# Kernel optimization log

Hardware: AMD Instinct MI355X
Metric: run time of the kernel (lower is better)

Reference implementation:

```python
import jax, jax.numpy as jnp
import numpy as np

NEG_SLOPE = 0.2
EPS = 1e-16


def add_self_loops(edge_index, num_nodes):
    loops = jnp.arange(num_nodes, dtype=edge_index.dtype)
    loops = jnp.stack([loops, loops])  # [2, N]
    return jnp.concatenate([edge_index, loops], axis=1)


def gat_conv(x, edge_index, W, att_src, att_dst, bias, heads, out_c, concat):
    # x: [N, F_in]; edge_index: [2, E] (src row 0 -> dst row 1)
    N = x.shape[0]
    h = (x @ W).reshape(N, heads, out_c)            # [N, H, C]
    src, dst = edge_index[0], edge_index[1]
    a_src = (h * att_src).sum(-1)                    # [N, H]
    a_dst = (h * att_dst).sum(-1)                    # [N, H]
    e = a_src[src] + a_dst[dst]                      # [E, H]
    e = jnp.where(e > 0, e, NEG_SLOPE * e)           # leaky_relu
    # segment softmax over destination node
    m = jax.ops.segment_max(e, dst, num_segments=N)  # [N, H]
    ex = jnp.exp(e - m[dst])                         # [E, H]
    denom = jax.ops.segment_sum(ex, dst, num_segments=N)  # [N, H]
    alpha = ex / (denom[dst] + EPS)                  # [E, H]
    msg = alpha[:, :, None] * h[src]                 # [E, H, C]
    out = jax.ops.segment_sum(msg, dst, num_segments=N)   # [N, H, C]
    if concat:
        out = out.reshape(N, heads * out_c)
    else:
        out = out.mean(axis=1)
    return out + bias


def setup_inputs() -> dict:
    key = jax.random.key(0)
    ks = jax.random.split(key, 12)
    N, E, F_IN, HID, H1, OUT = 100000, 1600000, 512, 8, 8, 40
    x = jax.random.normal(ks[0], (N, F_IN), dtype=jnp.float32)
    edge_index = jax.random.randint(ks[1], (2, E), 0, N, dtype=jnp.int64)
    glorot = lambda k, shp: jax.random.normal(k, shp, jnp.float32) * jnp.sqrt(2.0 / (shp[0] + shp[-1]))
    W1 = glorot(ks[2], (F_IN, H1 * HID))
    att_src1 = glorot(ks[3], (H1, HID))
    att_dst1 = glorot(ks[4], (H1, HID))
    b1 = jnp.zeros((H1 * HID,), jnp.float32)
    W2 = glorot(ks[5], (H1 * HID, 1 * OUT))
    att_src2 = glorot(ks[6], (1, OUT))
    att_dst2 = glorot(ks[7], (1, OUT))
    b2 = jnp.zeros((OUT,), jnp.float32)
    return {"x": x, "edge_index": edge_index, "W1": W1, "att_src1": att_src1,
            "att_dst1": att_dst1, "b1": b1, "W2": W2, "att_src2": att_src2,
            "att_dst2": att_dst2, "b2": b2}


def reference(x, edge_index, W1, att_src1, att_dst1, b1, W2, att_src2, att_dst2, b2):
    N = x.shape[0]
    ei = add_self_loops(edge_index, N)
    h = gat_conv(x, ei, W1, att_src1, att_dst1, b1, heads=8, out_c=8, concat=True)
    h = jax.nn.relu(h)
    # dropout p=0.0 / eval mode -> identity
    out = gat_conv(h, ei, W2, att_src2, att_dst2, b2, heads=1, out_c=40, concat=False)
    return jax.nn.log_softmax(out, axis=1)
```

## Files before the change

kernel.cpp:

```cpp
#include <hip/hip_runtime.h>
#include <math.h>

#define NEG_SLOPE 0.2f
#define EPS_DEN 1e-16f

__device__ __forceinline__ float leaky(float v) { return v > 0.f ? v : NEG_SLOPE * v; }

typedef __attribute__((ext_vector_type(8))) short bf16x8;
typedef __attribute__((ext_vector_type(4))) float f32x4;

__device__ __forceinline__ unsigned bf16rne(float f) {
    unsigned u = __float_as_uint(f);
    return (u + 0x7FFFu + ((u >> 16) & 1u)) >> 16;
}
__device__ __forceinline__ unsigned pack2(float a, float b) {
    unsigned r;
    asm("v_cvt_pk_bf16_f32 %0, %1, %2" : "=v"(r) : "v"(a), "v"(b));
    return r;
}
__device__ __forceinline__ float bfu(unsigned short u) {
    return __uint_as_float(((unsigned)u) << 16);
}

__global__ __launch_bounds__(256) void gemm1_mfma(
    const float* __restrict__ x, const float* __restrict__ W1,
    const float* __restrict__ att_src1, const float* __restrict__ att_dst1,
    unsigned short* __restrict__ h1b, float* __restrict__ a_src,
    float* __restrict__ a_dst, int N)
{
    __shared__ __align__(16) unsigned short As[128 * 40];
    __shared__ __align__(16) unsigned short Bs[64 * 40];

    const int t = threadIdx.x;
    const int w = t >> 6;
    const int lane = t & 63;
    const int m16 = lane & 15;
    const int quad = lane >> 4;
    const int rowBase = blockIdx.x * 128;

    f32x4 acc[2][4];
#pragma unroll
    for (int i = 0; i < 2; ++i)
#pragma unroll
        for (int j = 0; j < 4; ++j) acc[i][j] = (f32x4){0.f, 0.f, 0.f, 0.f};

    const float4* x4 = (const float4*)x;

#pragma unroll 1
    for (int chunk = 0; chunk < 16; ++chunk) {
        const int k0 = chunk * 32;
#pragma unroll
        for (int r = 0; r < 4; ++r) {
            int e = t + r * 256;
            int row = e >> 3;
            int kg = e & 7;
            int grow = rowBase + row;
            float4 v = make_float4(0.f, 0.f, 0.f, 0.f);
            if (grow < N) v = x4[(size_t)grow * 128 + (k0 >> 2) + kg];
            uint2 pk = make_uint2(pack2(v.x, v.y), pack2(v.z, v.w));
            *(uint2*)&As[row * 40 + kg * 4] = pk;
        }
        {
            int c = lane;
            int jb = w * 8;
            float f[8];
#pragma unroll
            for (int j = 0; j < 8; ++j) f[j] = W1[(size_t)(k0 + jb + j) * 64 + c];
            uint4 pk;
            pk.x = pack2(f[0], f[1]); pk.y = pack2(f[2], f[3]);
            pk.z = pack2(f[4], f[5]); pk.w = pack2(f[6], f[7]);
            *(uint4*)&Bs[c * 40 + jb] = pk;
        }
        __syncthreads();
        bf16x8 a0 = *(const bf16x8*)&As[(w * 32 + m16) * 40 + quad * 8];
        bf16x8 a1 = *(const bf16x8*)&As[(w * 32 + 16 + m16) * 40 + quad * 8];
#pragma unroll
        for (int j = 0; j < 4; ++j) {
            bf16x8 b = *(const bf16x8*)&Bs[(j * 16 + m16) * 40 + quad * 8];
            acc[0][j] = __builtin_amdgcn_mfma_f32_16x16x32_bf16(a0, b, acc[0][j], 0, 0, 0);
            acc[1][j] = __builtin_amdgcn_mfma_f32_16x16x32_bf16(a1, b, acc[1][j], 0, 0, 0);
        }
        __syncthreads();
    }

    float ats[4], atd[4];
#pragma unroll
    for (int j = 0; j < 4; ++j) {
        ats[j] = att_src1[j * 16 + m16];
        atd[j] = att_dst1[j * 16 + m16];
    }

#pragma unroll
    for (int i = 0; i < 2; ++i)
#pragma unroll
        for (int reg = 0; reg < 4; ++reg) {
            int r = rowBase + w * 32 + i * 16 + quad * 4 + reg;
            if (r < N) {
#pragma unroll
                for (int j = 0; j < 4; ++j) {
                    float val = acc[i][j][reg];
                    h1b[(size_t)r * 64 + j * 16 + m16] = (unsigned short)bf16rne(val);
                    float ps = val * ats[j];
                    float pd = val * atd[j];
                    ps += __shfl_xor(ps, 1); pd += __shfl_xor(pd, 1);
                    ps += __shfl_xor(ps, 2); pd += __shfl_xor(pd, 2);
                    ps += __shfl_xor(ps, 4); pd += __shfl_xor(pd, 4);
                    if ((m16 & 7) == 0) {
                        int head = j * 2 + (m16 >> 3);
                        a_src[(size_t)r * 8 + head] = ps;
                        a_dst[(size_t)r * 8 + head] = pd;
                    }
                }
            }
        }
}

__global__ __launch_bounds__(256) void deg_kernel(
    const int* __restrict__ ei, unsigned* __restrict__ deg, int E, int Etot)
{
    int idx = blockIdx.x * blockDim.x + threadIdx.x;
    if (idx >= Etot) return;
    int d = (idx < E) ? ei[E + idx] : (idx - E);
    atomicAdd(&deg[d], 1u);
}

__global__ __launch_bounds__(256) void scanA_kernel(
    const unsigned* __restrict__ deg, unsigned* __restrict__ loc,
    unsigned* __restrict__ bsum, int N)
{
    __shared__ unsigned sh[256];
    int i = blockIdx.x * 256 + threadIdx.x;
    unsigned v = (i < N) ? deg[i] : 0u;
    sh[threadIdx.x] = v;
    __syncthreads();
    for (int off = 1; off < 256; off <<= 1) {
        unsigned u = (threadIdx.x >= (unsigned)off) ? sh[threadIdx.x - off] : 0u;
        __syncthreads();
        sh[threadIdx.x] += u;
        __syncthreads();
    }
    if (i < N) loc[i] = sh[threadIdx.x] - v;
    if (threadIdx.x == 255) bsum[blockIdx.x] = sh[255];
}

__global__ __launch_bounds__(1024) void scanB_kernel(unsigned* __restrict__ bsum, int nb)
{
    __shared__ unsigned sh[1024];
    int t = threadIdx.x;
    unsigned carry = 0;
    for (int base = 0; base < nb; base += 1024) {
        int i = base + t;
        unsigned v = (i < nb) ? bsum[i] : 0u;
        sh[t] = v;
        __syncthreads();
        for (int off = 1; off < 1024; off <<= 1) {
            unsigned u = (t >= off) ? sh[t - off] : 0u;
            __syncthreads();
            sh[t] += u;
            __syncthreads();
        }
        unsigned incl = sh[t];
        unsigned tot  = sh[1023];
        __syncthreads();
        if (i < nb) bsum[i] = incl - v + carry;
        carry += tot;
        __syncthreads();
    }
}

__global__ __launch_bounds__(256) void scanC_kernel(
    const unsigned* __restrict__ loc, const unsigned* __restrict__ bsum,
    unsigned* __restrict__ rowstart, unsigned* __restrict__ cursor, int N, int Etot)
{
    int i = blockIdx.x * 256 + threadIdx.x;
    if (i >= N) return;
    unsigned r = loc[i] + bsum[blockIdx.x];
    rowstart[i] = r;
    cursor[i] = r;
    if (i == 0) rowstart[N] = (unsigned)Etot;
}

__global__ __launch_bounds__(256) void scatter_kernel(
    const int* __restrict__ ei, unsigned* __restrict__ cursor,
    int* __restrict__ csr_src, int E, int Etot, int sliceW)
{
    int slice = blockIdx.x & 7;
    int idx = (blockIdx.x >> 3) * 256 + threadIdx.x;
    if (idx >= Etot) return;
    int d = (idx < E) ? ei[E + idx] : (idx - E);
    int lo = slice * sliceW;
    if (d < lo || d >= lo + sliceW) return;
    int s = (idx < E) ? ei[idx] : d;
    unsigned pos = atomicAdd(&cursor[d], 1u);
    csr_src[pos] = s;
}

__global__ __launch_bounds__(256) void aggr1_kernel(
    const unsigned* __restrict__ rowstart, const int* __restrict__ csr_src,
    const float* __restrict__ a_src, const float* __restrict__ a_dst,
    const unsigned short* __restrict__ h1b, const float* __restrict__ b1,
    float* __restrict__ h2, int N)
{
    int g = blockIdx.x * 4 + (threadIdx.x >> 6);
    int lane = threadIdx.x & 63;
    if (g >= N) return;
    int half = lane >> 5;
    int l = lane & 31;
    int h = l >> 2;
    float ad = a_dst[(size_t)g * 8 + h];
    const unsigned* h1u = (const unsigned*)h1b;
    unsigned k0 = rowstart[g], k1 = rowstart[g + 1];
    float ax0 = 0.f, ay0 = 0.f, ax1 = 0.f, ay1 = 0.f;
    float dn0 = 0.f, dn1 = 0.f;
    unsigned k = k0;
    for (; k + 4 <= k1; k += 4) {
        int e0 = k + half, e1 = k + 2 + half;
        int s0 = csr_src[e0], s1 = csr_src[e1];
        float p0 = __expf(leaky(a_src[(size_t)s0 * 8 + h] + ad));
        float p1 = __expf(leaky(a_src[(size_t)s1 * 8 + h] + ad));
        unsigned v0 = h1u[(size_t)s0 * 32 + l];
        unsigned v1 = h1u[(size_t)s1 * 32 + l];
        ax0 += p0 * bfu((unsigned short)v0); ay0 += p0 * bfu((unsigned short)(v0 >> 16)); dn0 += p0;
        ax1 += p1 * bfu((unsigned short)v1); ay1 += p1 * bfu((unsigned short)(v1 >> 16)); dn1 += p1;
    }
    for (; k < k1; k += 2) {
        unsigned e = k + half;
        if (e < k1) {
            int s = csr_src[e];
            float p = __expf(leaky(a_src[(size_t)s * 8 + h] + ad));
            unsigned v = h1u[(size_t)s * 32 + l];
            ax0 += p * bfu((unsigned short)v); ay0 += p * bfu((unsigned short)(v >> 16)); dn0 += p;
        }
    }
    float ax = ax0 + ax1, ay = ay0 + ay1, dn = dn0 + dn1;
    ax += __shfl_xor(ax, 32);
    ay += __shfl_xor(ay, 32);
    dn += __shfl_xor(dn, 32);
    if (half == 0) {
        float inv = 1.f / (dn + EPS_DEN);
        float vx = ax * inv + b1[2 * l];
        float vy = ay * inv + b1[2 * l + 1];
        float2 o;
        o.x = vx > 0.f ? vx : 0.f;
        o.y = vy > 0.f ? vy : 0.f;
        *(float2*)&h2[(size_t)g * 64 + 2 * l] = o;
    }
}

__global__ __launch_bounds__(256) void gemm2_kernel(
    const float* __restrict__ h2, const float* __restrict__ W2,
    const float* __restrict__ att_src2, const float* __restrict__ att_dst2,
    unsigned short* __restrict__ h3b32, unsigned short* __restrict__ h3b8,
    float* __restrict__ a_src, float* __restrict__ a_dst, int N)
{
    __shared__ float Wl[64 * 40];
    int t = threadIdx.x;
    for (int i = t; i < 64 * 40; i += 256) Wl[i] = W2[i];
    __syncthreads();
    int lane = t & 63, wy = t >> 6;
    int row = blockIdx.x * 4 + wy;
    if (row >= N) return;
    float acc = 0.f;
    const float* hr = h2 + (size_t)row * 64;
    if (lane < 40) {
#pragma unroll 8
        for (int k = 0; k < 64; ++k) acc += hr[k] * Wl[k * 40 + lane];
        if (lane < 32) h3b32[(size_t)row * 32 + lane] = (unsigned short)bf16rne(acc);
        else           h3b8[(size_t)row * 8 + (lane - 32)] = (unsigned short)bf16rne(acc);
    }
    float ps = (lane < 40) ? acc * att_src2[lane] : 0.f;
    float pd = (lane < 40) ? acc * att_dst2[lane] : 0.f;
#pragma unroll
    for (int off = 32; off; off >>= 1) { ps += __shfl_down(ps, off); pd += __shfl_down(pd, off); }
    if (lane == 0) { a_src[row] = ps; a_dst[row] = pd; }
}

__global__ __launch_bounds__(256) void aggr2_kernel(
    const unsigned* __restrict__ rowstart, const int* __restrict__ csr_src,
    const float* __restrict__ a_src, const float* __restrict__ a_dst,
    const unsigned short* __restrict__ h3b32, const unsigned short* __restrict__ h3b8,
    const float* __restrict__ b2, float* __restrict__ y, int N)
{
    int g = blockIdx.x * 4 + (threadIdx.x >> 6);
    int lane = threadIdx.x & 63;
    if (g >= N) return;
    int half = lane >> 5;
    int l = lane & 31;
    const bool valid = l < 20;
    const unsigned* hsrc = (l < 16) ? (const unsigned*)h3b32 : (const unsigned*)h3b8;
    const int rowmul = (l < 16) ? 16 : 4;
    const int cidx   = (l < 16) ? l : (valid ? l - 16 : 0);
    float ad = a_dst[g];
    unsigned k0 = rowstart[g], k1 = rowstart[g + 1];
    float ax0 = 0.f, ay0 = 0.f, ax1 = 0.f, ay1 = 0.f;
    float dn0 = 0.f, dn1 = 0.f;
    unsigned k = k0;
    for (; k + 4 <= k1; k += 4) {
        int e0 = k + half, e1 = k + 2 + half;
        int s0 = csr_src[e0], s1 = csr_src[e1];
        float p0 = __expf(leaky(a_src[s0] + ad));
        float p1 = __expf(leaky(a_src[s1] + ad));
        unsigned v0 = valid ? hsrc[(size_t)s0 * rowmul + cidx] : 0u;
        unsigned v1 = valid ? hsrc[(size_t)s1 * rowmul + cidx] : 0u;
        ax0 += p0 * bfu((unsigned short)v0); ay0 += p0 * bfu((unsigned short)(v0 >> 16)); dn0 += p0;
        ax1 += p1 * bfu((unsigned short)v1); ay1 += p1 * bfu((unsigned short)(v1 >> 16)); dn1 += p1;
    }
    for (; k < k1; k += 2) {
        unsigned e = k + half;
        if (e < k1) {
            int s = csr_src[e];
            float p = __expf(leaky(a_src[s] + ad));
            unsigned v = valid ? hsrc[(size_t)s * rowmul + cidx] : 0u;
            ax0 += p * bfu((unsigned short)v); ay0 += p * bfu((unsigned short)(v >> 16)); dn0 += p;
        }
    }
    float ax = ax0 + ax1, ay = ay0 + ay1, dn = dn0 + dn1;
    ax += __shfl_xor(ax, 32);
    ay += __shfl_xor(ay, 32);
    dn += __shfl_xor(dn, 32);
    float inv = 1.f / (dn + EPS_DEN);
    float vx = valid ? (ax * inv + b2[2 * l]) : -INFINITY;
    float vy = valid ? (ay * inv + b2[2 * l + 1]) : -INFINITY;
    float mx = fmaxf(vx, vy);
#pragma unroll
    for (int off = 16; off; off >>= 1) mx = fmaxf(mx, __shfl_xor(mx, off));
    float ex = valid ? (__expf(vx - mx) + __expf(vy - mx)) : 0.f;
    float ss = ex;
#pragma unroll
    for (int off = 16; off; off >>= 1) ss += __shfl_xor(ss, off);
    float lse = mx + __logf(ss);
    if (half == 0 && valid) {
        float2 o;
        o.x = vx - lse;
        o.y = vy - lse;
        *(float2*)&y[(size_t)g * 40 + 2 * l] = o;
    }
}

extern "C" void kernel_launch(void* const* d_in, const int* in_sizes, int n_in,
                              void* d_out, int out_size, void* d_ws, size_t ws_size,
                              hipStream_t stream)
{
    const float* x        = (const float*)d_in[0];
    const int*   ei       = (const int*)d_in[1];
    const float* W1       = (const float*)d_in[2];
    const float* att_src1 = (const float*)d_in[3];
    const float* att_dst1 = (const float*)d_in[4];
    const float* b1       = (const float*)d_in[5];
    const float* W2       = (const float*)d_in[6];
    const float* att_src2 = (const float*)d_in[7];
    const float* att_dst2 = (const float*)d_in[8];
    const float* b2       = (const float*)d_in[9];
    float* y = (float*)d_out;

    int N = in_sizes[0] / 512;
    int E = in_sizes[1] / 2;
    int Etot = E + N;
    int nb = (N + 255) / 256;
    int sliceW = (N + 7) / 8;

    char* p = (char*)d_ws;
    unsigned short* h1b = (unsigned short*)p; p += (size_t)N * 64 * 2;
    float* a_src1a  = (float*)p;   p += (size_t)N * 8 * 4;
    float* a_dst1a  = (float*)p;   p += (size_t)N * 8 * 4;
    float* h2       = (float*)p;   p += (size_t)N * 64 * 4;
    unsigned short* h3b32 = (unsigned short*)p; p += (size_t)N * 32 * 2;
    unsigned short* h3b8  = (unsigned short*)p; p += (size_t)N * 8 * 2;
    float* a_src2a  = (float*)p;   p += (size_t)N * 4;
    float* a_dst2a  = (float*)p;   p += (size_t)N * 4;
    unsigned* deg   = (unsigned*)p; p += (size_t)N * 4;
    unsigned* loc   = (unsigned*)p; p += (size_t)N * 4;
    unsigned* bsum  = (unsigned*)p; p += (size_t)nb * 4;
    unsigned* rowstart = (unsigned*)p; p += (size_t)(N + 1) * 4;
    unsigned* cursor   = (unsigned*)p; p += (size_t)N * 4;
    int* csr_src    = (int*)p;     p += (size_t)Etot * 4;

    hipMemsetAsync(deg, 0, (size_t)N * 4, stream);

    gemm1_mfma<<<(N + 127) / 128, 256, 0, stream>>>(x, W1, att_src1, att_dst1, h1b, a_src1a, a_dst1a, N);

    deg_kernel<<<(Etot + 255) / 256, 256, 0, stream>>>(ei, deg, E, Etot);
    scanA_kernel<<<nb, 256, 0, stream>>>(deg, loc, bsum, N);
    scanB_kernel<<<1, 1024, 0, stream>>>(bsum, nb);
    scanC_kernel<<<nb, 256, 0, stream>>>(loc, bsum, rowstart, cursor, N, Etot);
    scatter_kernel<<<8 * ((Etot + 255) / 256), 256, 0, stream>>>(ei, cursor, csr_src, E, Etot, sliceW);

    aggr1_kernel<<<(N + 3) / 4, 256, 0, stream>>>(rowstart, csr_src, a_src1a, a_dst1a, h1b, b1, h2, N);

    gemm2_kernel<<<(N + 3) / 4, 256, 0, stream>>>(h2, W2, att_src2, att_dst2, h3b32, h3b8, a_src2a, a_dst2a, N);

    aggr2_kernel<<<(N + 3) / 4, 256, 0, stream>>>(rowstart, csr_src, a_src2a, a_dst2a, h3b32, h3b8, b2, y, N);
}
```

Before: 679.1 us.

## Prefetch next GEMM1 chunk into registers and unroll aggregation loops deeper

GEMM1 now loads the next K-chunk of x and W1 into registers while the MFMAs for the current chunk run, a register-level software pipeline meant to hide global load latency. Both aggregation kernels unroll the edge loop to 8 edges (4 per half-wave) with extra independent accumulators, so more gathers are in flight. Index arithmetic switches from 64-bit size_t to 32-bit unsigned to cut address computation cost. The costs are higher register pressure, possible lower occupancy, and a slightly different float summation order.

```diff
diff --git a/kernel.cpp b/kernel.cpp
--- a/kernel.cpp
+++ b/kernel.cpp
@@ -45,33 +45,56 @@
         for (int j = 0; j < 4; ++j) acc[i][j] = (f32x4){0.f, 0.f, 0.f, 0.f};
 
     const float4* x4 = (const float4*)x;
+    const int jb = w * 8;
+    const int c = lane;
+
+    int arow[4], akg[4], agrow[4];
+    bool aok[4];
+#pragma unroll
+    for (int r = 0; r < 4; ++r) {
+        int e = t + r * 256;
+        arow[r] = e >> 3;
+        akg[r] = e & 7;
+        agrow[r] = rowBase + arow[r];
+        aok[r] = agrow[r] < N;
+    }
+
+    float4 vx[4];
+    float wf[8];
+
+#pragma unroll
+    for (int r = 0; r < 4; ++r) {
+        vx[r] = make_float4(0.f, 0.f, 0.f, 0.f);
+        if (aok[r]) vx[r] = x4[(size_t)agrow[r] * 128 + akg[r]];
+    }
+#pragma unroll
+    for (int j = 0; j < 8; ++j) wf[j] = W1[(size_t)(jb + j) * 64 + c];
 
 #pragma unroll 1
     for (int chunk = 0; chunk < 16; ++chunk) {
-        const int k0 = chunk * 32;
 #pragma unroll
         for (int r = 0; r < 4; ++r) {
-            int e = t + r * 256;
-            int row = e >> 3;
-            int kg = e & 7;
-            int grow = rowBase + row;
-            float4 v = make_float4(0.f, 0.f, 0.f, 0.f);
-            if (grow < N) v = x4[(size_t)grow * 128 + (k0 >> 2) + kg];
-            uint2 pk = make_uint2(pack2(v.x, v.y), pack2(v.z, v.w));
-            *(uint2*)&As[row * 40 + kg * 4] = pk;
+            uint2 pk = make_uint2(pack2(vx[r].x, vx[r].y), pack2(vx[r].z, vx[r].w));
+            *(uint2*)&As[arow[r] * 40 + akg[r] * 4] = pk;
         }
         {
-            int c = lane;
-            int jb = w * 8;
-            float f[8];
-#pragma unroll
-            for (int j = 0; j < 8; ++j) f[j] = W1[(size_t)(k0 + jb + j) * 64 + c];
             uint4 pk;
-            pk.x = pack2(f[0], f[1]); pk.y = pack2(f[2], f[3]);
-            pk.z = pack2(f[4], f[5]); pk.w = pack2(f[6], f[7]);
+            pk.x = pack2(wf[0], wf[1]); pk.y = pack2(wf[2], wf[3]);
+            pk.z = pack2(wf[4], wf[5]); pk.w = pack2(wf[6], wf[7]);
             *(uint4*)&Bs[c * 40 + jb] = pk;
         }
         __syncthreads();
+
+        if (chunk < 15) {
+            const int k0n = (chunk + 1) * 32;
+#pragma unroll
+            for (int r = 0; r < 4; ++r) {
+                if (aok[r]) vx[r] = x4[(size_t)agrow[r] * 128 + (k0n >> 2) + akg[r]];
+            }
+#pragma unroll
+            for (int j = 0; j < 8; ++j) wf[j] = W1[(size_t)(k0n + jb + j) * 64 + c];
+        }
+
         bf16x8 a0 = *(const bf16x8*)&As[(w * 32 + m16) * 40 + quad * 8];
         bf16x8 a1 = *(const bf16x8*)&As[(w * 32 + 16 + m16) * 40 + quad * 8];
 #pragma unroll
@@ -211,15 +234,34 @@
     const unsigned* h1u = (const unsigned*)h1b;
     unsigned k0 = rowstart[g], k1 = rowstart[g + 1];
     float ax0 = 0.f, ay0 = 0.f, ax1 = 0.f, ay1 = 0.f;
-    float dn0 = 0.f, dn1 = 0.f;
+    float ax2 = 0.f, ay2 = 0.f, ax3 = 0.f, ay3 = 0.f;
+    float dn0 = 0.f, dn1 = 0.f, dn2 = 0.f, dn3 = 0.f;
     unsigned k = k0;
+    for (; k + 8 <= k1; k += 8) {
+        int s0 = csr_src[k + half];
+        int s1 = csr_src[k + 2 + half];
+        int s2 = csr_src[k + 4 + half];
+        int s3 = csr_src[k + 6 + half];
+        float p0 = __expf(leaky(a_src[(unsigned)s0 * 8u + h] + ad));
+        float p1 = __expf(leaky(a_src[(unsigned)s1 * 8u + h] + ad));
+        float p2 = __expf(leaky(a_src[(unsigned)s2 * 8u + h] + ad));
+        float p3 = __expf(leaky(a_src[(unsigned)s3 * 8u + h] + ad));
+        unsigned v0 = h1u[(unsigned)s0 * 32u + l];
+        unsigned v1 = h1u[(unsigned)s1 * 32u + l];
+        unsigned v2 = h1u[(unsigned)s2 * 32u + l];
+        unsigned v3 = h1u[(unsigned)s3 * 32u + l];
+        ax0 += p0 * bfu((unsigned short)v0); ay0 += p0 * bfu((unsigned short)(v0 >> 16)); dn0 += p0;
+        ax1 += p1 * bfu((unsigned short)v1); ay1 += p1 * bfu((unsigned short)(v1 >> 16)); dn1 += p1;
+        ax2 += p2 * bfu((unsigned short)v2); ay2 += p2 * bfu((unsigned short)(v2 >> 16)); dn2 += p2;
+        ax3 += p3 * bfu((unsigned short)v3); ay3 += p3 * bfu((unsigned short)(v3 >> 16)); dn3 += p3;
+    }
     for (; k + 4 <= k1; k += 4) {
-        int e0 = k + half, e1 = k + 2 + half;
-        int s0 = csr_src[e0], s1 = csr_src[e1];
-        float p0 = __expf(leaky(a_src[(size_t)s0 * 8 + h] + ad));
-        float p1 = __expf(leaky(a_src[(size_t)s1 * 8 + h] + ad));
-        unsigned v0 = h1u[(size_t)s0 * 32 + l];
-        unsigned v1 = h1u[(size_t)s1 * 32 + l];
+        int s0 = csr_src[k + half];
+        int s1 = csr_src[k + 2 + half];
+        float p0 = __expf(leaky(a_src[(unsigned)s0 * 8u + h] + ad));
+        float p1 = __expf(leaky(a_src[(unsigned)s1 * 8u + h] + ad));
+        unsigned v0 = h1u[(unsigned)s0 * 32u + l];
+        unsigned v1 = h1u[(unsigned)s1 * 32u + l];
         ax0 += p0 * bfu((unsigned short)v0); ay0 += p0 * bfu((unsigned short)(v0 >> 16)); dn0 += p0;
         ax1 += p1 * bfu((unsigned short)v1); ay1 += p1 * bfu((unsigned short)(v1 >> 16)); dn1 += p1;
     }
@@ -227,12 +269,14 @@
         unsigned e = k + half;
         if (e < k1) {
             int s = csr_src[e];
-            float p = __expf(leaky(a_src[(size_t)s * 8 + h] + ad));
-            unsigned v = h1u[(size_t)s * 32 + l];
+            float p = __expf(leaky(a_src[(unsigned)s * 8u + h] + ad));
+            unsigned v = h1u[(unsigned)s * 32u + l];
             ax0 += p * bfu((unsigned short)v); ay0 += p * bfu((unsigned short)(v >> 16)); dn0 += p;
         }
     }
-    float ax = ax0 + ax1, ay = ay0 + ay1, dn = dn0 + dn1;
+    float ax = (ax0 + ax1) + (ax2 + ax3);
+    float ay = (ay0 + ay1) + (ay2 + ay3);
+    float dn = (dn0 + dn1) + (dn2 + dn3);
     ax += __shfl_xor(ax, 32);
     ay += __shfl_xor(ay, 32);
     dn += __shfl_xor(dn, 32);
@@ -288,20 +332,39 @@
     int l = lane & 31;
     const bool valid = l < 20;
     const unsigned* hsrc = (l < 16) ? (const unsigned*)h3b32 : (const unsigned*)h3b8;
-    const int rowmul = (l < 16) ? 16 : 4;
-    const int cidx   = (l < 16) ? l : (valid ? l - 16 : 0);
+    const unsigned rowmul = (l < 16) ? 16u : 4u;
+    const unsigned cidx   = (l < 16) ? (unsigned)l : (valid ? (unsigned)(l - 16) : 0u);
     float ad = a_dst[g];
     unsigned k0 = rowstart[g], k1 = rowstart[g + 1];
     float ax0 = 0.f, ay0 = 0.f, ax1 = 0.f, ay1 = 0.f;
-    float dn0 = 0.f, dn1 = 0.f;
+    float ax2 = 0.f, ay2 = 0.f, ax3 = 0.f, ay3 = 0.f;
+    float dn0 = 0.f, dn1 = 0.f, dn2 = 0.f, dn3 = 0.f;
     unsigned k = k0;
-    for (; k + 4 <= k1; k += 4) {
-        int e0 = k + half, e1 = k + 2 + half;
-        int s0 = csr_src[e0], s1 = csr_src[e1];
+    for (; k + 8 <= k1; k += 8) {
+        int s0 = csr_src[k + half];
+        int s1 = csr_src[k + 2 + half];
+        int s2 = csr_src[k + 4 + half];
+        int s3 = csr_src[k + 6 + half];
         float p0 = __expf(leaky(a_src[s0] + ad));
         float p1 = __expf(leaky(a_src[s1] + ad));
-        unsigned v0 = valid ? hsrc[(size_t)s0 * rowmul + cidx] : 0u;
-        unsigned v1 = valid ? hsrc[(size_t)s1 * rowmul + cidx] : 0u;
+        float p2 = __expf(leaky(a_src[s2] + ad));
+        float p3 = __expf(leaky(a_src[s3] + ad));
+        unsigned v0 = valid ? hsrc[(unsigned)s0 * rowmul + cidx] : 0u;
+        unsigned v1 = valid ? hsrc[(unsigned)s1 * rowmul + cidx] : 0u;
+        unsigned v2 = valid ? hsrc[(unsigned)s2 * rowmul + cidx] : 0u;
+        unsigned v3 = valid ? hsrc[(unsigned)s3 * rowmul + cidx] : 0u;
+        ax0 += p0 * bfu((unsigned short)v0); ay0 += p0 * bfu((unsigned short)(v0 >> 16)); dn0 += p0;
+        ax1 += p1 * bfu((unsigned short)v1); ay1 += p1 * bfu((unsigned short)(v1 >> 16)); dn1 += p1;
+        ax2 += p2 * bfu((unsigned short)v2); ay2 += p2 * bfu((unsigned short)(v2 >> 16)); dn2 += p2;
+        ax3 += p3 * bfu((unsigned short)v3); ay3 += p3 * bfu((unsigned short)(v3 >> 16)); dn3 += p3;
+    }
+    for (; k + 4 <= k1; k += 4) {
+        int s0 = csr_src[k + half];
+        int s1 = csr_src[k + 2 + half];
+        float p0 = __expf(leaky(a_src[s0] + ad));
+        float p1 = __expf(leaky(a_src[s1] + ad));
+        unsigned v0 = valid ? hsrc[(unsigned)s0 * rowmul + cidx] : 0u;
+        unsigned v1 = valid ? hsrc[(unsigned)s1 * rowmul + cidx] : 0u;
         ax0 += p0 * bfu((unsigned short)v0); ay0 += p0 * bfu((unsigned short)(v0 >> 16)); dn0 += p0;
         ax1 += p1 * bfu((unsigned short)v1); ay1 += p1 * bfu((unsigned short)(v1 >> 16)); dn1 += p1;
     }
@@ -310,11 +373,13 @@
         if (e < k1) {
             int s = csr_src[e];
             float p = __expf(leaky(a_src[s] + ad));
-            unsigned v = valid ? hsrc[(size_t)s * rowmul + cidx] : 0u;
+            unsigned v = valid ? hsrc[(unsigned)s * rowmul + cidx] : 0u;
             ax0 += p * bfu((unsigned short)v); ay0 += p * bfu((unsigned short)(v >> 16)); dn0 += p;
         }
     }
-    float ax = ax0 + ax1, ay = ay0 + ay1, dn = dn0 + dn1;
+    float ax = (ax0 + ax1) + (ax2 + ax3);
+    float ay = (ay0 + ay1) + (ay2 + ay3);
+    float dn = (dn0 + dn1) + (dn2 + dn3);
     ax += __shfl_xor(ax, 32);
     ay += __shfl_xor(ay, 32);
     dn += __shfl_xor(dn, 32);
```

Result: faster. 659.2 us (-2.9%).
